# Performance work log

Measured on AMD Instinct MI355X. Metric: run time of the kernel, lower is better.

## Reference

```python
import jax, jax.numpy as jnp
import numpy as np

B, L, NS, NW, D = 65536, 64, 32, 256, 8
ALPHA = 0.6  # hard-coded in affine_coupling.call


def setup_inputs() -> dict:
    key = jax.random.key(0)
    ks = jax.random.split(key, 12)
    return {
        "x": jax.random.normal(ks[0], (B, L), jnp.float32),
        "logdet": jnp.zeros((B, 1), jnp.float32),
        # actnorm params (b_init/logs_init are zero since data_init=True)
        "b": jax.random.normal(ks[1], (D, 1, L), jnp.float32) * 0.05,
        "logs": jax.random.normal(ks[2], (D, 1, L), jnp.float32) * 0.05,
        # NN2 params per depth: Dense(32->256), Dense(256->256), Dense(256->64)
        "W1": jax.random.normal(ks[3], (D, NS, NW), jnp.float32) / np.sqrt(NS),
        "b1": jax.random.normal(ks[4], (D, NW), jnp.float32) * 0.01,
        "W2": jax.random.normal(ks[5], (D, NW, NW), jnp.float32) / np.sqrt(NW),
        "b2": jax.random.normal(ks[6], (D, NW), jnp.float32) * 0.01,
        "Wf": jax.random.normal(ks[7], (D, NW, 2 * (L - NS)), jnp.float32) / np.sqrt(NW),
        "bf": jax.random.normal(ks[8], (D, 2 * (L - NS)), jnp.float32) * 0.01,
        "log_gamma": jax.random.normal(ks[9], (D, 1, L - NS), jnp.float32) * 0.05,
    }


def reference(x, logdet, b, logs, W1, b1, W2, b2, Wf, bf, log_gamma):
    z = x
    for i in range(D):  # fixed small depth loop over structurally distinct params
        # actnorm (forward): x = (z + b) * exp(logs); logdet += sum(logs)
        z = (z + b[i]) * jnp.exp(logs[i])
        logdet = logdet + jnp.sum(logs[i])
        # affine coupling (flow_coupling=1), split at NS (constant for L=2*NS)
        z1, z2 = z[:, :NS], z[:, NS:]
        h = jax.nn.relu(z1 @ W1[i] + b1[i])
        h = jax.nn.relu(h @ W2[i] + b2[i])
        h = h @ Wf[i] + bf[i]  # [B, 2*(L-NS)]
        shift = jnp.exp(log_gamma[i]) * jnp.tanh(h[:, ::2])
        scale = ALPHA * jnp.tanh(h[:, 1::2])
        z2 = z2 + scale * z2 + shift
        logdet = logdet + jnp.sum(jnp.log1p(scale), axis=1, keepdims=True)
        # concat then channel reversal z[:, ::-1]
        z = jnp.concatenate([z1, z2], axis=1)[:, ::-1]
    return z, logdet
```

## Files before the change

### kernel.cpp

```cpp
#include <hip/hip_runtime.h>
#include <math.h>

#define BB 65536
#define ND 8

typedef float f4 __attribute__((ext_vector_type(4)));
typedef float f32x4 __attribute__((ext_vector_type(4)));
typedef _Float16 half8 __attribute__((ext_vector_type(8)));
typedef __fp16 fp16x2 __attribute__((ext_vector_type(2)));

#define F1_OFF 0
#define F2_OFF 131072
#define F3_OFF 1179648
#define WTOT_F16 1441792

#define MFMA16(a, b, c) __builtin_amdgcn_mfma_f32_16x16x32_f16((a), (b), (c), 0, 0, 0)

__global__ __launch_bounds__(256)
void prep_weights(const float* __restrict__ W1, const float* __restrict__ W2,
                  const float* __restrict__ Wf, _Float16* __restrict__ wt)
{
    int t = blockIdx.x * 256 + threadIdx.x;
    float wv;
    int p;
    if (t < F2_OFF) {
        int rec = t >> 9, off = t & 511;
        p = rec & 1;
        int nt = (rec >> 1) & 15, i = rec >> 5;
        int l = off >> 3, j = off & 7;
        int n = nt*16 + (l & 15), k = (l >> 4)*8 + j;
        wv = W1[i*8192 + k*256 + n];
    } else if (t < F3_OFF) {
        int u = t - F2_OFF;
        int rec = u >> 9, off = u & 511;
        p = rec & 1;
        int nt = (rec >> 1) & 15, ks = (rec >> 5) & 7, i = rec >> 8;
        int l = off >> 3, j = off & 7;
        int n = nt*16 + (l & 15), k = ks*32 + (l >> 4)*8 + j;
        wv = W2[i*65536 + k*256 + n];
    } else {
        int u = t - F3_OFF;
        int rec = u >> 9, off = u & 511;
        p = rec & 1;
        int nt = (rec >> 1) & 3, ks = (rec >> 3) & 7, i = rec >> 6;
        int l = off >> 3, j = off & 7;
        int n = nt*16 + (l & 15), k = ks*32 + (l >> 4)*8 + j;
        wv = Wf[i*16384 + k*64 + n];
    }
    _Float16 hi = (_Float16)wv;
    wt[t] = p ? (_Float16)(wv - (float)hi) : hi;
}

__device__ __forceinline__ void split8(f4 a, f4 b, half8& hi, half8& lo)
{
    union U { half8 v; fp16x2 h[4]; } H, L;
    H.h[0] = __builtin_amdgcn_cvt_pkrtz(a[0], a[1]);
    H.h[1] = __builtin_amdgcn_cvt_pkrtz(a[2], a[3]);
    H.h[2] = __builtin_amdgcn_cvt_pkrtz(b[0], b[1]);
    H.h[3] = __builtin_amdgcn_cvt_pkrtz(b[2], b[3]);
    L.h[0] = __builtin_amdgcn_cvt_pkrtz(a[0] - (float)H.h[0][0], a[1] - (float)H.h[0][1]);
    L.h[1] = __builtin_amdgcn_cvt_pkrtz(a[2] - (float)H.h[1][0], a[3] - (float)H.h[1][1]);
    L.h[2] = __builtin_amdgcn_cvt_pkrtz(b[0] - (float)H.h[2][0], b[1] - (float)H.h[2][1]);
    L.h[3] = __builtin_amdgcn_cvt_pkrtz(b[2] - (float)H.h[3][0], b[3] - (float)H.h[3][1]);
    hi = H.v; lo = L.v;
}

__global__ __launch_bounds__(256, 2)
void flow_mfma(const float* __restrict__ x,
               const float* __restrict__ logdet_in,
               const float* __restrict__ bP,
               const float* __restrict__ logsP,
               const float* __restrict__ b1P,
               const float* __restrict__ b2P,
               const float* __restrict__ bfP,
               const float* __restrict__ lgP,
               const _Float16* __restrict__ wt,
               float* __restrict__ out)
{
    __shared__ float zb[64 * 64];
    __shared__ float hb[64 * 256];

    const int tid  = threadIdx.x;
    const int w    = tid >> 6;
    const int wr   = w >> 1;
    const int wc   = w & 1;
    const int lane = tid & 63;
    const int li   = lane & 15;
    const int lg4  = lane >> 4;
    const int row0 = blockIdx.x * 64;

    float lsum;
    {
        float s = 0.f;
        #pragma unroll
        for (int i2 = 0; i2 < 8; ++i2) s += logsP[i2*64 + lane];
        s += __shfl_xor(s, 1);  s += __shfl_xor(s, 2);  s += __shfl_xor(s, 4);
        s += __shfl_xor(s, 8);  s += __shfl_xor(s, 16); s += __shfl_xor(s, 32);
        lsum = s;
    }

    {
        const f4* xs = (const f4*)(x + (size_t)row0 * 64);
        #pragma unroll
        for (int q = 0; q < 4; ++q) {
            int idx4 = tid + q*256;
            int r = idx4 >> 4, cf = idx4 & 15;
            *(f4*)&zb[r*64 + ((cf ^ (r & 7)) << 2)] = xs[idx4];
        }
    }

    const int rA = (wr*2 + 0)*16 + li;
    const int rB = (wr*2 + 1)*16 + li;
    const int sA = rA & 7, sB = rB & 7;

    float ldp0 = 0.f, ldp1 = 0.f;
    const f32x4 zero4 = {0.f, 0.f, 0.f, 0.f};

    #pragma unroll 1
    for (int i = 0; i < ND; ++i) {
        __syncthreads();

        #pragma unroll
        for (int q = 0; q < 4; ++q) {
            int idx4 = tid + q*256;
            int r = idx4 >> 4, cf = idx4 & 15;
            float* zp = &zb[r*64 + ((cf ^ (r & 7)) << 2)];
            f4 z  = *(f4*)zp;
            f4 bv = *(const f4*)&bP[i*64 + cf*4];
            f4 lv = *(const f4*)&logsP[i*64 + cf*4];
            f4 ev = { __expf(lv[0]), __expf(lv[1]), __expf(lv[2]), __expf(lv[3]) };
            z = (z + bv) * ev;
            *(f4*)zp = z;
        }
        __syncthreads();

        {
            half8 bh0, bl0, bh1, bl1;
            {
                int cf = lg4 * 2;
                f4 a0 = *(const f4*)&zb[rA*64 + (((cf    ) ^ sA) << 2)];
                f4 a1 = *(const f4*)&zb[rA*64 + (((cf + 1) ^ sA) << 2)];
                split8(a0, a1, bh0, bl0);
                f4 c0 = *(const f4*)&zb[rB*64 + (((cf    ) ^ sB) << 2)];
                f4 c1 = *(const f4*)&zb[rB*64 + (((cf + 1) ^ sB) << 2)];
                split8(c0, c1, bh1, bl1);
            }
            f32x4 acc[8][2];
            #pragma unroll
            for (int nt = 0; nt < 8; ++nt) { acc[nt][0] = zero4; acc[nt][1] = zero4; }
            const _Float16* w1f = wt + F1_OFF + i*16384 + lane*8;
            #pragma unroll
            for (int nt = 0; nt < 8; ++nt) {
                const _Float16* fb = w1f + (wc*8 + nt)*1024;
                half8 ah = *(const half8*)fb;
                half8 al = *(const half8*)(fb + 512);
                acc[nt][0] = MFMA16(ah, bh0, acc[nt][0]);
                acc[nt][1] = MFMA16(ah, bh1, acc[nt][1]);
                acc[nt][0] = MFMA16(ah, bl0, acc[nt][0]);
                acc[nt][1] = MFMA16(ah, bl1, acc[nt][1]);
                acc[nt][0] = MFMA16(al, bh0, acc[nt][0]);
                acc[nt][1] = MFMA16(al, bh1, acc[nt][1]);
            }
            const float* bb = b1P + i*256;
            #pragma unroll
            for (int nt = 0; nt < 8; ++nt) {
                int n0 = wc*128 + nt*16 + lg4*4;
                f4 bias = *(const f4*)&bb[n0];
                int cfw = n0 >> 2;
                #pragma unroll
                for (int rt = 0; rt < 2; ++rt) {
                    int r  = rt ? rB : rA;
                    int sr = rt ? sB : sA;
                    f4 v = acc[nt][rt] + bias;
                    v[0] = fmaxf(v[0], 0.f); v[1] = fmaxf(v[1], 0.f);
                    v[2] = fmaxf(v[2], 0.f); v[3] = fmaxf(v[3], 0.f);
                    *(f4*)&hb[r*256 + ((cfw ^ sr) << 2)] = v;
                }
            }
        }
        __syncthreads();

        {
            f32x4 acc[8][2];
            #pragma unroll
            for (int nt = 0; nt < 8; ++nt) { acc[nt][0] = zero4; acc[nt][1] = zero4; }
            const _Float16* w2f = wt + F2_OFF + i*131072 + lane*8;
            #pragma unroll 2
            for (int ks = 0; ks < 8; ++ks) {
                int cf = ks*8 + lg4*2;
                half8 ph0, pl0, ph1, pl1;
                f4 a0 = *(const f4*)&hb[rA*256 + (((cf    ) ^ sA) << 2)];
                f4 a1 = *(const f4*)&hb[rA*256 + (((cf + 1) ^ sA) << 2)];
                split8(a0, a1, ph0, pl0);
                f4 c0 = *(const f4*)&hb[rB*256 + (((cf    ) ^ sB) << 2)];
                f4 c1 = *(const f4*)&hb[rB*256 + (((cf + 1) ^ sB) << 2)];
                split8(c0, c1, ph1, pl1);
                const _Float16* wk = w2f + ks*16384;
                #pragma unroll
                for (int nt = 0; nt < 8; ++nt) {
                    const _Float16* fb = wk + (wc*8 + nt)*1024;
                    half8 ah = *(const half8*)fb;
                    half8 al = *(const half8*)(fb + 512);
                    acc[nt][0] = MFMA16(ah, ph0, acc[nt][0]);
                    acc[nt][1] = MFMA16(ah, ph1, acc[nt][1]);
                    acc[nt][0] = MFMA16(ah, pl0, acc[nt][0]);
                    acc[nt][1] = MFMA16(ah, pl1, acc[nt][1]);
                    acc[nt][0] = MFMA16(al, ph0, acc[nt][0]);
                    acc[nt][1] = MFMA16(al, ph1, acc[nt][1]);
                }
            }
            __syncthreads();
            const float* bb = b2P + i*256;
            #pragma unroll
            for (int nt = 0; nt < 8; ++nt) {
                int n0 = wc*128 + nt*16 + lg4*4;
                f4 bias = *(const f4*)&bb[n0];
                int cfw = n0 >> 2;
                #pragma unroll
                for (int rt = 0; rt < 2; ++rt) {
                    int r  = rt ? rB : rA;
                    int sr = rt ? sB : sA;
                    f4 v = acc[nt][rt] + bias;
                    v[0] = fmaxf(v[0], 0.f); v[1] = fmaxf(v[1], 0.f);
                    v[2] = fmaxf(v[2], 0.f); v[3] = fmaxf(v[3], 0.f);
                    *(f4*)&hb[r*256 + ((cfw ^ sr) << 2)] = v;
                }
            }
        }
        __syncthreads();

        {
            f32x4 acc[2][2];
            acc[0][0] = zero4; acc[0][1] = zero4; acc[1][0] = zero4; acc[1][1] = zero4;
            const _Float16* w3f = wt + F3_OFF + i*32768 + lane*8;
            #pragma unroll 2
            for (int ks = 0; ks < 8; ++ks) {
                int cf = ks*8 + lg4*2;
                half8 ph0, pl0, ph1, pl1;
                f4 a0 = *(const f4*)&hb[rA*256 + (((cf    ) ^ sA) << 2)];
                f4 a1 = *(const f4*)&hb[rA*256 + (((cf + 1) ^ sA) << 2)];
                split8(a0, a1, ph0, pl0);
                f4 c0 = *(const f4*)&hb[rB*256 + (((cf    ) ^ sB) << 2)];
                f4 c1 = *(const f4*)&hb[rB*256 + (((cf + 1) ^ sB) << 2)];
                split8(c0, c1, ph1, pl1);
                const _Float16* wk = w3f + ks*4096;
                #pragma unroll
                for (int nt = 0; nt < 2; ++nt) {
                    const _Float16* fb = wk + (wc*2 + nt)*1024;
                    half8 ah = *(const half8*)fb;
                    half8 al = *(const half8*)(fb + 512);
                    acc[nt][0] = MFMA16(ah, ph0, acc[nt][0]);
                    acc[nt][1] = MFMA16(ah, ph1, acc[nt][1]);
                    acc[nt][0] = MFMA16(ah, pl0, acc[nt][0]);
                    acc[nt][1] = MFMA16(ah, pl1, acc[nt][1]);
                    acc[nt][0] = MFMA16(al, ph0, acc[nt][0]);
                    acc[nt][1] = MFMA16(al, ph1, acc[nt][1]);
                }
            }
            #pragma unroll
            for (int nt = 0; nt < 2; ++nt) {
                int n0 = (wc*2 + nt)*16 + lg4*4;
                int j0 = n0 >> 1;
                f4 bias = *(const f4*)&bfP[i*64 + n0];
                float eg0 = __expf(lgP[i*32 + j0]);
                float eg1 = __expf(lgP[i*32 + j0 + 1]);
                #pragma unroll
                for (int rt = 0; rt < 2; ++rt) {
                    int r  = rt ? rB : rA;
                    int sr = rt ? sB : sA;
                    f4 v = acc[nt][rt];
                    float sh0 = eg0  * tanhf(v[0] + bias[0]);
                    float sc0 = 0.6f * tanhf(v[1] + bias[1]);
                    float sh1 = eg1  * tanhf(v[2] + bias[2]);
                    float sc1 = 0.6f * tanhf(v[3] + bias[3]);
                    int c = 32 + j0;
                    int addr = r*64 + ((((c >> 2) ^ sr)) << 2) + (c & 3);
                    float z0  = zb[addr];
                    float z1v = zb[addr + 1];
                    zb[addr]     = fmaf(sc0, z0,  z0  + sh0);
                    zb[addr + 1] = fmaf(sc1, z1v, z1v + sh1);
                    float l01 = log1pf(sc0) + log1pf(sc1);
                    if (rt == 0) ldp0 += l01; else ldp1 += l01;
                }
            }
        }
        __syncthreads();

        #pragma unroll
        for (int q = 0; q < 2; ++q) {
            int task = tid + q*256;
            int r = task >> 3, cfL = task & 7;
            int s = r & 7;
            float* pL = &zb[r*64 + ((cfL ^ s) << 2)];
            float* pR = &zb[r*64 + (((15 - cfL) ^ s) << 2)];
            f4 Lv = *(f4*)pL;
            f4 Rv = *(f4*)pR;
            f4 nL = { Rv[3], Rv[2], Rv[1], Rv[0] };
            f4 nR = { Lv[3], Lv[2], Lv[1], Lv[0] };
            *(f4*)pL = nL;
            *(f4*)pR = nR;
        }
    }
    __syncthreads();

    {
        f4* oz = (f4*)(out + (size_t)row0 * 64);
        #pragma unroll
        for (int q = 0; q < 4; ++q) {
            int idx4 = tid + q*256;
            int r = idx4 >> 4, cf = idx4 & 15;
            oz[idx4] = *(const f4*)&zb[r*64 + ((cf ^ (r & 7)) << 2)];
        }
    }

    float v0 = ldp0 + __shfl_xor(ldp0, 16); v0 += __shfl_xor(v0, 32);
    float v1 = ldp1 + __shfl_xor(ldp1, 16); v1 += __shfl_xor(v1, 32);
    if (lg4 == 0) {
        hb[rA*2 + wc] = v0;
        hb[rB*2 + wc] = v1;
    }
    __syncthreads();
    if (tid < 64) {
        int gr = row0 + tid;
        out[(size_t)BB * 64 + gr] = logdet_in[gr] + lsum + hb[tid*2] + hb[tid*2 + 1];
    }
}

extern "C" void kernel_launch(void* const* d_in, const int* in_sizes, int n_in,
                              void* d_out, int out_size, void* d_ws, size_t ws_size,
                              hipStream_t stream)
{
    const float* x    = (const float*)d_in[0];
    const float* ld   = (const float*)d_in[1];
    const float* b    = (const float*)d_in[2];
    const float* logs = (const float*)d_in[3];
    const float* W1   = (const float*)d_in[4];
    const float* b1   = (const float*)d_in[5];
    const float* W2   = (const float*)d_in[6];
    const float* b2   = (const float*)d_in[7];
    const float* Wf   = (const float*)d_in[8];
    const float* bf   = (const float*)d_in[9];
    const float* lg   = (const float*)d_in[10];
    _Float16* wt = (_Float16*)d_ws;
    float* out = (float*)d_out;

    prep_weights<<<WTOT_F16 / 256, 256, 0, stream>>>(W1, W2, Wf, wt);
    flow_mfma<<<1024, 256, 0, stream>>>(x, ld, b, logs, b1, b2, bf, lg, wt, out);
}
```

Measured before the change: 433.3 us.

## Halve rows per block, split N across four waves, raise occupancy, fast tanh/log

Each block now handles 32 rows instead of 64. The four waves split the output columns rather than a 2x2 row/column grid, which halves the accumulator registers and shared memory per block. Launch bounds rise to 4 blocks per CU and the grid doubles to 2048 blocks. The aim is more resident waves to hide latency. The cost is that each weight fragment is reloaded for fewer rows, roughly doubling weight traffic from cache. tanhf and log1pf in the epilogue are replaced with exp/log-based fast approximations, which slightly reduce accuracy.

```diff
diff --git a/kernel.cpp b/kernel.cpp
--- a/kernel.cpp
+++ b/kernel.cpp
@@ -65,7 +65,14 @@
     hi = H.v; lo = L.v;
 }
 
-__global__ __launch_bounds__(256, 2)
+__device__ __forceinline__ float fast_tanh(float x)
+{
+    float e = __expf(2.0f * fabsf(x));
+    float t = 1.0f - 2.0f / (e + 1.0f);
+    return copysignf(t, x);
+}
+
+__global__ __launch_bounds__(256, 4)
 void flow_mfma(const float* __restrict__ x,
                const float* __restrict__ logdet_in,
                const float* __restrict__ bP,
@@ -77,17 +84,15 @@
                const _Float16* __restrict__ wt,
                float* __restrict__ out)
 {
-    __shared__ float zb[64 * 64];
-    __shared__ float hb[64 * 256];
+    __shared__ float zb[32 * 64];
+    __shared__ float hb[32 * 256];
 
     const int tid  = threadIdx.x;
     const int w    = tid >> 6;
-    const int wr   = w >> 1;
-    const int wc   = w & 1;
     const int lane = tid & 63;
     const int li   = lane & 15;
     const int lg4  = lane >> 4;
-    const int row0 = blockIdx.x * 64;
+    const int row0 = blockIdx.x * 32;
 
     float lsum;
     {
@@ -102,16 +107,16 @@
     {
         const f4* xs = (const f4*)(x + (size_t)row0 * 64);
         #pragma unroll
-        for (int q = 0; q < 4; ++q) {
+        for (int q = 0; q < 2; ++q) {
             int idx4 = tid + q*256;
             int r = idx4 >> 4, cf = idx4 & 15;
             *(f4*)&zb[r*64 + ((cf ^ (r & 7)) << 2)] = xs[idx4];
         }
     }
 
-    const int rA = (wr*2 + 0)*16 + li;
-    const int rB = (wr*2 + 1)*16 + li;
-    const int sA = rA & 7, sB = rB & 7;
+    const int rA = li;
+    const int rB = 16 + li;
+    const int s8 = li & 7;
 
     float ldp0 = 0.f, ldp1 = 0.f;
     const f32x4 zero4 = {0.f, 0.f, 0.f, 0.f};
@@ -121,7 +126,7 @@
         __syncthreads();
 
         #pragma unroll
-        for (int q = 0; q < 4; ++q) {
+        for (int q = 0; q < 2; ++q) {
             int idx4 = tid + q*256;
             int r = idx4 >> 4, cf = idx4 & 15;
             float* zp = &zb[r*64 + ((cf ^ (r & 7)) << 2)];
@@ -138,20 +143,20 @@
             half8 bh0, bl0, bh1, bl1;
             {
                 int cf = lg4 * 2;
-                f4 a0 = *(const f4*)&zb[rA*64 + (((cf    ) ^ sA) << 2)];
-                f4 a1 = *(const f4*)&zb[rA*64 + (((cf + 1) ^ sA) << 2)];
+                f4 a0 = *(const f4*)&zb[rA*64 + (((cf    ) ^ s8) << 2)];
+                f4 a1 = *(const f4*)&zb[rA*64 + (((cf + 1) ^ s8) << 2)];
                 split8(a0, a1, bh0, bl0);
-                f4 c0 = *(const f4*)&zb[rB*64 + (((cf    ) ^ sB) << 2)];
-                f4 c1 = *(const f4*)&zb[rB*64 + (((cf + 1) ^ sB) << 2)];
+                f4 c0 = *(const f4*)&zb[rB*64 + (((cf    ) ^ s8) << 2)];
+                f4 c1 = *(const f4*)&zb[rB*64 + (((cf + 1) ^ s8) << 2)];
                 split8(c0, c1, bh1, bl1);
             }
-            f32x4 acc[8][2];
-            #pragma unroll
-            for (int nt = 0; nt < 8; ++nt) { acc[nt][0] = zero4; acc[nt][1] = zero4; }
+            f32x4 acc[4][2];
+            #pragma unroll
+            for (int nt = 0; nt < 4; ++nt) { acc[nt][0] = zero4; acc[nt][1] = zero4; }
             const _Float16* w1f = wt + F1_OFF + i*16384 + lane*8;
             #pragma unroll
-            for (int nt = 0; nt < 8; ++nt) {
-                const _Float16* fb = w1f + (wc*8 + nt)*1024;
+            for (int nt = 0; nt < 4; ++nt) {
+                const _Float16* fb = w1f + (w*4 + nt)*1024;
                 half8 ah = *(const half8*)fb;
                 half8 al = *(const half8*)(fb + 512);
                 acc[nt][0] = MFMA16(ah, bh0, acc[nt][0]);
@@ -163,42 +168,41 @@
             }
             const float* bb = b1P + i*256;
             #pragma unroll
-            for (int nt = 0; nt < 8; ++nt) {
-                int n0 = wc*128 + nt*16 + lg4*4;
+            for (int nt = 0; nt < 4; ++nt) {
+                int n0 = w*64 + nt*16 + lg4*4;
                 f4 bias = *(const f4*)&bb[n0];
                 int cfw = n0 >> 2;
                 #pragma unroll
                 for (int rt = 0; rt < 2; ++rt) {
-                    int r  = rt ? rB : rA;
-                    int sr = rt ? sB : sA;
+                    int r = rt ? rB : rA;
                     f4 v = acc[nt][rt] + bias;
                     v[0] = fmaxf(v[0], 0.f); v[1] = fmaxf(v[1], 0.f);
                     v[2] = fmaxf(v[2], 0.f); v[3] = fmaxf(v[3], 0.f);
-                    *(f4*)&hb[r*256 + ((cfw ^ sr) << 2)] = v;
+                    *(f4*)&hb[r*256 + ((cfw ^ s8) << 2)] = v;
                 }
             }
         }
         __syncthreads();
 
         {
-            f32x4 acc[8][2];
-            #pragma unroll
-            for (int nt = 0; nt < 8; ++nt) { acc[nt][0] = zero4; acc[nt][1] = zero4; }
+            f32x4 acc[4][2];
+            #pragma unroll
+            for (int nt = 0; nt < 4; ++nt) { acc[nt][0] = zero4; acc[nt][1] = zero4; }
             const _Float16* w2f = wt + F2_OFF + i*131072 + lane*8;
             #pragma unroll 2
             for (int ks = 0; ks < 8; ++ks) {
                 int cf = ks*8 + lg4*2;
                 half8 ph0, pl0, ph1, pl1;
-                f4 a0 = *(const f4*)&hb[rA*256 + (((cf    ) ^ sA) << 2)];
-                f4 a1 = *(const f4*)&hb[rA*256 + (((cf + 1) ^ sA) << 2)];
+                f4 a0 = *(const f4*)&hb[rA*256 + (((cf    ) ^ s8) << 2)];
+                f4 a1 = *(const f4*)&hb[rA*256 + (((cf + 1) ^ s8) << 2)];
                 split8(a0, a1, ph0, pl0);
-                f4 c0 = *(const f4*)&hb[rB*256 + (((cf    ) ^ sB) << 2)];
-                f4 c1 = *(const f4*)&hb[rB*256 + (((cf + 1) ^ sB) << 2)];
+                f4 c0 = *(const f4*)&hb[rB*256 + (((cf    ) ^ s8) << 2)];
+                f4 c1 = *(const f4*)&hb[rB*256 + (((cf + 1) ^ s8) << 2)];
                 split8(c0, c1, ph1, pl1);
                 const _Float16* wk = w2f + ks*16384;
                 #pragma unroll
-                for (int nt = 0; nt < 8; ++nt) {
-                    const _Float16* fb = wk + (wc*8 + nt)*1024;
+                for (int nt = 0; nt < 4; ++nt) {
+                    const _Float16* fb = wk + (w*4 + nt)*1024;
                     half8 ah = *(const half8*)fb;
                     half8 al = *(const half8*)(fb + 512);
                     acc[nt][0] = MFMA16(ah, ph0, acc[nt][0]);
@@ -212,84 +216,75 @@
             __syncthreads();
             const float* bb = b2P + i*256;
             #pragma unroll
-            for (int nt = 0; nt < 8; ++nt) {
-                int n0 = wc*128 + nt*16 + lg4*4;
+            for (int nt = 0; nt < 4; ++nt) {
+                int n0 = w*64 + nt*16 + lg4*4;
                 f4 bias = *(const f4*)&bb[n0];
                 int cfw = n0 >> 2;
                 #pragma unroll
                 for (int rt = 0; rt < 2; ++rt) {
-                    int r  = rt ? rB : rA;
-                    int sr = rt ? sB : sA;
+                    int r = rt ? rB : rA;
                     f4 v = acc[nt][rt] + bias;
                     v[0] = fmaxf(v[0], 0.f); v[1] = fmaxf(v[1], 0.f);
                     v[2] = fmaxf(v[2], 0.f); v[3] = fmaxf(v[3], 0.f);
-                    *(f4*)&hb[r*256 + ((cfw ^ sr) << 2)] = v;
+                    *(f4*)&hb[r*256 + ((cfw ^ s8) << 2)] = v;
                 }
             }
         }
         __syncthreads();
 
         {
-            f32x4 acc[2][2];
-            acc[0][0] = zero4; acc[0][1] = zero4; acc[1][0] = zero4; acc[1][1] = zero4;
+            f32x4 acc3[2];
+            acc3[0] = zero4; acc3[1] = zero4;
             const _Float16* w3f = wt + F3_OFF + i*32768 + lane*8;
             #pragma unroll 2
             for (int ks = 0; ks < 8; ++ks) {
                 int cf = ks*8 + lg4*2;
                 half8 ph0, pl0, ph1, pl1;
-                f4 a0 = *(const f4*)&hb[rA*256 + (((cf    ) ^ sA) << 2)];
-                f4 a1 = *(const f4*)&hb[rA*256 + (((cf + 1) ^ sA) << 2)];
+                f4 a0 = *(const f4*)&hb[rA*256 + (((cf    ) ^ s8) << 2)];
+                f4 a1 = *(const f4*)&hb[rA*256 + (((cf + 1) ^ s8) << 2)];
                 split8(a0, a1, ph0, pl0);
-                f4 c0 = *(const f4*)&hb[rB*256 + (((cf    ) ^ sB) << 2)];
-                f4 c1 = *(const f4*)&hb[rB*256 + (((cf + 1) ^ sB) << 2)];
+                f4 c0 = *(const f4*)&hb[rB*256 + (((cf    ) ^ s8) << 2)];
+                f4 c1 = *(const f4*)&hb[rB*256 + (((cf + 1) ^ s8) << 2)];
                 split8(c0, c1, ph1, pl1);
-                const _Float16* wk = w3f + ks*4096;
-                #pragma unroll
-                for (int nt = 0; nt < 2; ++nt) {
-                    const _Float16* fb = wk + (wc*2 + nt)*1024;
-                    half8 ah = *(const half8*)fb;
-                    half8 al = *(const half8*)(fb + 512);
-                    acc[nt][0] = MFMA16(ah, ph0, acc[nt][0]);
-                    acc[nt][1] = MFMA16(ah, ph1, acc[nt][1]);
-                    acc[nt][0] = MFMA16(ah, pl0, acc[nt][0]);
-                    acc[nt][1] = MFMA16(ah, pl1, acc[nt][1]);
-                    acc[nt][0] = MFMA16(al, ph0, acc[nt][0]);
-                    acc[nt][1] = MFMA16(al, ph1, acc[nt][1]);
-                }
-            }
-            #pragma unroll
-            for (int nt = 0; nt < 2; ++nt) {
-                int n0 = (wc*2 + nt)*16 + lg4*4;
+                const _Float16* fb = w3f + ks*4096 + w*1024;
+                half8 ah = *(const half8*)fb;
+                half8 al = *(const half8*)(fb + 512);
+                acc3[0] = MFMA16(ah, ph0, acc3[0]);
+                acc3[1] = MFMA16(ah, ph1, acc3[1]);
+                acc3[0] = MFMA16(ah, pl0, acc3[0]);
+                acc3[1] = MFMA16(ah, pl1, acc3[1]);
+                acc3[0] = MFMA16(al, ph0, acc3[0]);
+                acc3[1] = MFMA16(al, ph1, acc3[1]);
+            }
+            {
+                int n0 = w*16 + lg4*4;
                 int j0 = n0 >> 1;
                 f4 bias = *(const f4*)&bfP[i*64 + n0];
                 float eg0 = __expf(lgP[i*32 + j0]);
                 float eg1 = __expf(lgP[i*32 + j0 + 1]);
                 #pragma unroll
                 for (int rt = 0; rt < 2; ++rt) {
-                    int r  = rt ? rB : rA;
-                    int sr = rt ? sB : sA;
-                    f4 v = acc[nt][rt];
-                    float sh0 = eg0  * tanhf(v[0] + bias[0]);
-                    float sc0 = 0.6f * tanhf(v[1] + bias[1]);
-                    float sh1 = eg1  * tanhf(v[2] + bias[2]);
-                    float sc1 = 0.6f * tanhf(v[3] + bias[3]);
+                    int r = rt ? rB : rA;
+                    f4 v = acc3[rt];
+                    float sh0 = eg0  * fast_tanh(v[0] + bias[0]);
+                    float sc0 = 0.6f * fast_tanh(v[1] + bias[1]);
+                    float sh1 = eg1  * fast_tanh(v[2] + bias[2]);
+                    float sc1 = 0.6f * fast_tanh(v[3] + bias[3]);
                     int c = 32 + j0;
-                    int addr = r*64 + ((((c >> 2) ^ sr)) << 2) + (c & 3);
+                    int addr = r*64 + ((((c >> 2) ^ s8)) << 2) + (c & 3);
                     float z0  = zb[addr];
                     float z1v = zb[addr + 1];
                     zb[addr]     = fmaf(sc0, z0,  z0  + sh0);
                     zb[addr + 1] = fmaf(sc1, z1v, z1v + sh1);
-                    float l01 = log1pf(sc0) + log1pf(sc1);
+                    float l01 = __logf(1.0f + sc0) + __logf(1.0f + sc1);
                     if (rt == 0) ldp0 += l01; else ldp1 += l01;
                 }
             }
         }
         __syncthreads();
 
-        #pragma unroll
-        for (int q = 0; q < 2; ++q) {
-            int task = tid + q*256;
-            int r = task >> 3, cfL = task & 7;
+        {
+            int r = tid >> 3, cfL = tid & 7;
             int s = r & 7;
             float* pL = &zb[r*64 + ((cfL ^ s) << 2)];
             float* pR = &zb[r*64 + (((15 - cfL) ^ s) << 2)];
@@ -306,7 +301,7 @@
     {
         f4* oz = (f4*)(out + (size_t)row0 * 64);
         #pragma unroll
-        for (int q = 0; q < 4; ++q) {
+        for (int q = 0; q < 2; ++q) {
             int idx4 = tid + q*256;
             int r = idx4 >> 4, cf = idx4 & 15;
             oz[idx4] = *(const f4*)&zb[r*64 + ((cf ^ (r & 7)) << 2)];
@@ -316,13 +311,14 @@
     float v0 = ldp0 + __shfl_xor(ldp0, 16); v0 += __shfl_xor(v0, 32);
     float v1 = ldp1 + __shfl_xor(ldp1, 16); v1 += __shfl_xor(v1, 32);
     if (lg4 == 0) {
-        hb[rA*2 + wc] = v0;
-        hb[rB*2 + wc] = v1;
+        hb[rA*4 + w] = v0;
+        hb[rB*4 + w] = v1;
     }
     __syncthreads();
-    if (tid < 64) {
+    if (tid < 32) {
         int gr = row0 + tid;
-        out[(size_t)BB * 64 + gr] = logdet_in[gr] + lsum + hb[tid*2] + hb[tid*2 + 1];
+        out[(size_t)BB * 64 + gr] = logdet_in[gr] + lsum
+                                  + hb[tid*4] + hb[tid*4+1] + hb[tid*4+2] + hb[tid*4+3];
     }
 }
 
@@ -345,5 +341,5 @@
     float* out = (float*)d_out;
 
     prep_weights<<<WTOT_F16 / 256, 256, 0, stream>>>(W1, W2, Wf, wt);
-    flow_mfma<<<1024, 256, 0, stream>>>(x, ld, b, logs, b1, b2, bf, lg, wt, out);
-}
+    flow_mfma<<<2048, 256, 0, stream>>>(x, ld, b, logs, b1, b2, bf, lg, wt, out);
+}
```

Result: no change. 435.9 us (+0.6%).
